# Kernel tuning notes

Hardware: AMD Instinct MI355X
Metric: run time of the kernel (lower is better)

The kernel has to match this reference:

```python
import jax, jax.numpy as jnp
import numpy as np
from jax import lax


def _batch_conv(x, w, b):
    # x: [B, Cin, H, W], w: [B, Cout, Cin, kh, kw], b: [B, Cout]
    # Per-sample conv (the torch code's groups=B grouped-conv trick),
    # expressed as vmap over the batch of an ordinary conv.
    def one(xi, wi):
        return lax.conv_general_dilated(
            xi[None], wi, window_strides=(1, 1), padding='SAME',
            dimension_numbers=('NCHW', 'OIHW', 'NCHW'))[0]
    y = jax.vmap(one)(x, w)                       # [B, Cout, H, W]
    return y + b[:, :, None, None]


def setup_inputs() -> dict:
    key = jax.random.key(0)
    ks = jax.random.split(key, 9)
    B, Cin, H, W = 32, 3, 64, 64
    NC = 10
    s = 0.05
    return {
        'x': jax.random.normal(ks[0], (B, Cin, H, W), jnp.float32),
        'conv1_weight': jax.random.normal(ks[1], (B, 64, Cin, 3, 3), jnp.float32) * s,
        'conv2_weight': jax.random.normal(ks[2], (B, 128, 64, 3, 3), jnp.float32) * s,
        'conv3_weight': jax.random.normal(ks[3], (B, 256, 128, 3, 3), jnp.float32) * s,
        'fc_weight': jax.random.normal(ks[4], (B, 1, NC), jnp.float32) * s,
        'bias1': jax.random.normal(ks[5], (B, 64), jnp.float32) * s,
        'bias2': jax.random.normal(ks[6], (B, 128), jnp.float32) * s,
        'bias3': jax.random.normal(ks[7], (B, 256), jnp.float32) * s,
        'bias4': jax.random.normal(ks[8], (B, NC), jnp.float32) * s,
    }


def reference(x, conv1_weight, conv2_weight, conv3_weight, fc_weight,
              bias1, bias2, bias3, bias4):
    h = jax.nn.relu(_batch_conv(x, conv1_weight, bias1))   # [B, 64, H, W]
    h = jax.nn.relu(_batch_conv(h, conv2_weight, bias2))   # [B, 128, H, W]
    h = jax.nn.relu(_batch_conv(h, conv3_weight, bias3))   # [B, 256, H, W]
    h = jnp.mean(h, axis=(2, 3))                           # AdaptiveAvgPool2d(1) -> [B, 256]
    h = h[:, :, None]                                      # view(B, N, -1) -> [B, 256, 1]
    # BatchLinearLayer: bmm(x, weight) + bias
    out = jnp.einsum('bnd,bdo->bno', h, fc_weight) + bias4[:, None, :]  # [B, 256, 10]
    return out
```

## Files before the change

### kernel.cpp

```cpp
#include <hip/hip_runtime.h>
#include <stdint.h>

typedef __attribute__((ext_vector_type(8))) short short8;
typedef __attribute__((ext_vector_type(16))) float f32x16;

#define NB 32

__device__ __forceinline__ float bf2f(uint16_t v) {
    return __uint_as_float(((uint32_t)v) << 16);
}
__device__ __forceinline__ uint16_t f2bf(float f) {
    uint32_t u = __float_as_uint(f);
    u += 0x7fffu + ((u >> 16) & 1u);
    return (uint16_t)(u >> 16);
}

__device__ __forceinline__ void gload16(const void* g, void* l) {
    __builtin_amdgcn_global_load_lds(
        (const __attribute__((address_space(1))) uint32_t*)g,
        (__attribute__((address_space(3))) uint32_t*)l, 16, 0, 0);
}

template<int COUT, int CIN>
__device__ __forceinline__ void prep_w_item(int idx, const float* __restrict__ w,
                                            uint16_t* __restrict__ wp)
{
    const int ci = idx % CIN;
    const int t  = idx / CIN;
    const int oc = t % COUT;
    const int b  = t / COUT;
    const float* s = w + (size_t)idx * 9;
    #pragma unroll
    for (int k = 0; k < 9; k++)
        wp[((size_t)(b * 9 + k) * COUT + oc) * CIN + ci] = f2bf(s[k]);
}

__global__ __launch_bounds__(256) void prep_w3_k(
    const float* __restrict__ w, uint16_t* __restrict__ wp)
{
    const int idx = blockIdx.x * 256 + threadIdx.x;
    if (idx < NB * 256 * 128) prep_w_item<256, 128>(idx, w, wp);
}

template<bool DO_W3>
__global__ __launch_bounds__(256) void prep_all(
    const float* __restrict__ x,  const float* __restrict__ w1,
    const float* __restrict__ w2, const float* __restrict__ w3,
    uint16_t* __restrict__ xp,  uint16_t* __restrict__ wp1,
    uint16_t* __restrict__ wp2, uint16_t* __restrict__ wp3,
    float* __restrict__ zp)
{
    int idx = blockIdx.x * 256 + threadIdx.x;
    if (idx < 4096) {
        ((float4*)zp)[idx] = make_float4(0.f, 0.f, 0.f, 0.f);
        return;
    }
    idx -= 4096;
    if (idx < 131072) {
        const int xc = idx & 63, y = (idx >> 6) & 63, b = idx >> 12;
        const float* s = x + (size_t)b * 3 * 4096 + y * 64 + xc;
        const uint16_t v0 = f2bf(s[0]), v1 = f2bf(s[4096]), v2 = f2bf(s[8192]);
        short8 lo = {(short)v0, (short)v1, (short)v2, 0, 0, 0, 0, 0};
        short8 hi = {0, 0, 0, 0, 0, 0, 0, 0};
        uint16_t* d = xp + (size_t)idx * 16;
        *(short8*)d = lo;
        *(short8*)(d + 8) = hi;
        return;
    }
    idx -= 131072;
    if (idx < 18432) {
        const int oc = idx & 63, k = (idx >> 6) % 9, b = idx / 576;
        const uint16_t v0 = f2bf(w1[((size_t)(b * 64 + oc) * 3 + 0) * 9 + k]);
        const uint16_t v1 = f2bf(w1[((size_t)(b * 64 + oc) * 3 + 1) * 9 + k]);
        const uint16_t v2 = f2bf(w1[((size_t)(b * 64 + oc) * 3 + 2) * 9 + k]);
        short8 lo = {(short)v0, (short)v1, (short)v2, 0, 0, 0, 0, 0};
        short8 hi = {0, 0, 0, 0, 0, 0, 0, 0};
        uint16_t* d = wp1 + ((size_t)(b * 9 + k) * 64 + oc) * 16;
        *(short8*)d = lo;
        *(short8*)(d + 8) = hi;
        return;
    }
    idx -= 18432;
    if (idx < 262144) {
        prep_w_item<128, 64>(idx, w2, wp2);
        return;
    }
    if (!DO_W3) return;
    idx -= 262144;
    if (idx < 1048576) prep_w_item<256, 128>(idx, w3, wp3);
}

template<int CIN, int COUT, int OCBLKS, bool POOL>
__global__ __launch_bounds__(512, 4) void conv_mfma(
    const uint16_t* __restrict__ in, const uint16_t* __restrict__ wp,
    const float* __restrict__ bias, uint16_t* __restrict__ out,
    float* __restrict__ partial, const float* __restrict__ zp)
{
    constexpr int IN_CH = 21;
    constexpr int W_CH  = 18;
    constexpr int IN_B  = IN_CH * 1024;
    constexpr int BUF_B = IN_B + W_CH * 1024;
    constexpr int P     = OCBLKS * 8;
    extern __shared__ __align__(16) char sm[];

    const int L   = blockIdx.x;
    const int xcd = L & 7;
    const int jj  = L >> 3;
    const int b   = (jj / P) * 8 + xcd;
    const int inner = jj % P;
    const int ocbase = (inner >> 3) * 64;
    const int stripe = inner & 7;
    const int y0 = stripe * 8;

    const int tid = threadIdx.x;
    const int w  = tid >> 6;
    const int wv = w >> 1, h = w & 1;
    const int l  = tid & 63, q = l >> 5, ln = l & 31;
    const int NK = CIN / 16;

    const uint16_t* srcp[5];
    int ldsoff[5];
    #pragma unroll
    for (int j = 0; j < 5; j++) {
        const int chunk = w * 5 + j;
        if (chunk >= IN_CH + W_CH) {
            srcp[j] = (const uint16_t*)zp;
            ldsoff[j] = -1;
        } else if (chunk < IN_CH) {
            const int gp = chunk * 64 + l;
            const int rq = gp / 66, px = gp - rq * 66;
            const int row = rq >> 1, qq = rq & 1;
            const int gy = y0 - 1 + row, gx = px - 1;
            const bool valid = (rq < 20) && ((unsigned)gy < 64u) && ((unsigned)gx < 64u);
            srcp[j] = valid ? in + ((size_t)((b * 64 + gy) * 64 + gx) * CIN + qq * 8)
                            : (const uint16_t*)zp;
            ldsoff[j] = chunk * 1024;
        } else {
            const int c2 = chunk - IN_CH;
            const int kk = c2 >> 1, qq = c2 & 1, oc = l;
            srcp[j] = wp + ((size_t)(b * 9 + kk) * COUT + ocbase + oc) * CIN + qq * 8;
            ldsoff[j] = IN_B + c2 * 1024;
        }
    }

    int aoffA[4];
    #pragma unroll
    for (int t = 0; t < 4; t++)
        aoffA[t] = ((((wv * 2 + t) * 2 + q) * 66) + h * 32 + ln) * 16;
    const int boffB = q * 1024 + ln * 16;

    f32x16 aA0, aA1, aC0, aC1;
    {
        const float bv0 = bias[b * COUT + ocbase + ln];
        const float bv1 = bias[b * COUT + ocbase + 32 + ln];
        #pragma unroll
        for (int r = 0; r < 16; r++) {
            aA0[r] = bv0; aC0[r] = bv0;
            aA1[r] = bv1; aC1[r] = bv1;
        }
    }

    auto stage = [&](int bufsel, int k) {
        const int koff = k * 16;
        char* base = sm + bufsel * BUF_B;
        #pragma unroll
        for (int j = 0; j < 5; j++) {
            char* dst = (ldsoff[j] < 0) ? (sm + 2 * BUF_B)
                                        : (base + ldsoff[j]);
            gload16(srcp[j] + koff, dst);
        }
    };

    stage(0, 0);
    if (NK > 1) stage(1, 1);

    for (int k = 0; k < NK; k++) {
        const char* cb = sm + (k & 1) * BUF_B;
        if (k + 1 < NK) asm volatile("s_waitcnt vmcnt(5)" ::: "memory");
        else            asm volatile("s_waitcnt vmcnt(0)" ::: "memory");
        __builtin_amdgcn_s_barrier();
        __builtin_amdgcn_sched_barrier(0);
        __builtin_amdgcn_s_setprio(1);
        #pragma unroll
        for (int kx = 0; kx < 3; kx++) {
            short8 fA[4];
            #pragma unroll
            for (int t = 0; t < 4; t++)
                fA[t] = *(const short8*)(cb + aoffA[t] + kx * 16);
            #pragma unroll
            for (int ky = 0; ky < 3; ky++) {
                const int kk = ky * 3 + kx;
                const char* bw = cb + IN_B + kk * 2048 + boffB;
                short8 b0 = *(const short8*)(bw);
                short8 b1 = *(const short8*)(bw + 512);
                aA0 = __builtin_amdgcn_mfma_f32_32x32x16_bf16(fA[ky], b0, aA0, 0, 0, 0);
                aA1 = __builtin_amdgcn_mfma_f32_32x32x16_bf16(fA[ky], b1, aA1, 0, 0, 0);
                aC0 = __builtin_amdgcn_mfma_f32_32x32x16_bf16(fA[ky + 1], b0, aC0, 0, 0, 0);
                aC1 = __builtin_amdgcn_mfma_f32_32x32x16_bf16(fA[ky + 1], b1, aC1, 0, 0, 0);
            }
        }
        __builtin_amdgcn_s_setprio(0);
        __builtin_amdgcn_s_barrier();
        if (k + 2 < NK) stage(k & 1, k + 2);
    }

    if (!POOL) {
        #pragma unroll
        for (int r = 0; r < 16; r++) {
            const int pxr = h * 32 + (r & 3) + 8 * (r >> 2) + 4 * q;
            const int y0w = y0 + wv * 2;
            uint16_t* dA = out + (size_t)((b * 64 + y0w) * 64 + pxr) * COUT + ocbase;
            uint16_t* dC = out + (size_t)((b * 64 + y0w + 1) * 64 + pxr) * COUT + ocbase;
            dA[ln]      = f2bf(fmaxf(aA0[r], 0.f));
            dA[32 + ln] = f2bf(fmaxf(aA1[r], 0.f));
            dC[ln]      = f2bf(fmaxf(aC0[r], 0.f));
            dC[32 + ln] = f2bf(fmaxf(aC1[r], 0.f));
        }
    } else {
        float* red = (float*)(sm + 2 * BUF_B);
        float s0 = 0.f, s1 = 0.f;
        #pragma unroll
        for (int r = 0; r < 16; r++) {
            s0 += fmaxf(aA0[r], 0.f) + fmaxf(aC0[r], 0.f);
            s1 += fmaxf(aA1[r], 0.f) + fmaxf(aC1[r], 0.f);
        }
        s0 += __shfl_xor(s0, 32);
        s1 += __shfl_xor(s1, 32);
        __syncthreads();
        if (q == 0) {
            red[w * 64 + ln] = s0;
            red[w * 64 + 32 + ln] = s1;
        }
        __syncthreads();
        if (tid < 64) {
            float t = 0.f;
            #pragma unroll
            for (int i = 0; i < 8; i++) t += red[i * 64 + tid];
            partial[(size_t)(b * 256 + ocbase + tid) * 8 + stripe] = t;
        }
    }
}

__global__ void fc_k(const float* __restrict__ partial,
                     const float* __restrict__ fcw,
                     const float* __restrict__ b4, float* __restrict__ out)
{
    const int b = blockIdx.x, c = threadIdx.x;
    const float* p = partial + (size_t)(b * 256 + c) * 8;
    float s = 0.f;
    #pragma unroll
    for (int i = 0; i < 8; i++) s += p[i];
    const float pooled = s * (1.f / 4096.f);
    #pragma unroll
    for (int o = 0; o < 10; o++)
        out[(b * 256 + c) * 10 + o] = fmaf(pooled, fcw[b * 10 + o], b4[b * 10 + o]);
}

extern "C" void kernel_launch(void* const* d_in, const int* in_sizes, int n_in,
                              void* d_out, int out_size, void* d_ws, size_t ws_size,
                              hipStream_t stream)
{
    const float* x   = (const float*)d_in[0];
    const float* w1  = (const float*)d_in[1];
    const float* w2  = (const float*)d_in[2];
    const float* w3  = (const float*)d_in[3];
    const float* fcw = (const float*)d_in[4];
    const float* b1  = (const float*)d_in[5];
    const float* b2  = (const float*)d_in[6];
    const float* b3  = (const float*)d_in[7];
    const float* b4  = (const float*)d_in[8];
    char* ws = (char*)d_ws;
    uint16_t* xp  = (uint16_t*)(ws);
    uint16_t* wp1 = (uint16_t*)(ws + 4194304);
    uint16_t* h2  = (uint16_t*)(ws);
    uint16_t* h1  = (uint16_t*)(ws + 33554432);
    uint16_t* wp2 = (uint16_t*)(ws + 50331648);
    const bool big_ws = ws_size >= 74186752u;
    uint16_t* wp3     = (uint16_t*)(ws + (big_ws ? 55050240u : 33554432u));
    float*    partial = (float*)   (ws + (big_ws ? 73924608u : 52428800u));
    float*    zp      = (float*)d_out;

    constexpr int DYN_LDS = 2 * 39936 + 2048;
    static bool attr_done = false;
    if (!attr_done) {
        hipFuncSetAttribute((const void*)&conv_mfma<16, 64, 1, false>,
                            hipFuncAttributeMaxDynamicSharedMemorySize, DYN_LDS);
        hipFuncSetAttribute((const void*)&conv_mfma<64, 128, 2, false>,
                            hipFuncAttributeMaxDynamicSharedMemorySize, DYN_LDS);
        hipFuncSetAttribute((const void*)&conv_mfma<128, 256, 4, true>,
                            hipFuncAttributeMaxDynamicSharedMemorySize, DYN_LDS);
        attr_done = true;
    }

    if (big_ws) {
        prep_all<true><<<5720, 256, 0, stream>>>(x, w1, w2, w3, xp, wp1, wp2, wp3, zp);
    } else {
        prep_all<false><<<1624, 256, 0, stream>>>(x, w1, w2, w3, xp, wp1, wp2, wp3, zp);
    }
    conv_mfma<16, 64, 1, false><<<NB * 8, 512, DYN_LDS, stream>>>(xp, wp1, b1, h1, nullptr, zp);
    conv_mfma<64, 128, 2, false><<<NB * 16, 512, DYN_LDS, stream>>>(h1, wp2, b2, h2, nullptr, zp);
    if (!big_ws)
        prep_w3_k<<<4096, 256, 0, stream>>>(w3, wp3);
    conv_mfma<128, 256, 4, true><<<NB * 32, 512, DYN_LDS, stream>>>(h2, wp3, b3, nullptr, partial, zp);
    fc_k<<<NB, 256, 0, stream>>>(partial, fcw, b4, (float*)d_out);
}
```

Before: 133.8 us.

## Retile conv kernels so each block covers all output channels of a 4-row stripe

The conv kernel is restructured so each 256-thread block computes every output channel for a 4-row stripe, instead of a 64-channel slice of an 8-row stripe. Each wave now holds a 4xNF grid of MFMA accumulators, which gives more reuse of each A and B fragment per LDS read. The K loop now walks (ky, channel-chunk) phases with smaller double-buffered LDS tiles, and the next kx fragments are prefetched into registers. This aims to cut redundant input loads across channel blocks and raise MFMA density. The cost is fewer blocks and waves per CU (launch_bounds 256,1), much higher register pressure for NF=4, and a per-phase full vmcnt(0) wait with a barrier.

```diff
diff --git a/kernel.cpp b/kernel.cpp
--- a/kernel.cpp
+++ b/kernel.cpp
@@ -6,9 +6,6 @@
 
 #define NB 32
 
-__device__ __forceinline__ float bf2f(uint16_t v) {
-    return __uint_as_float(((uint32_t)v) << 16);
-}
 __device__ __forceinline__ uint16_t f2bf(float f) {
     uint32_t u = __float_as_uint(f);
     u += 0x7fffu + ((u >> 16) & 1u);
@@ -90,153 +87,186 @@
     if (idx < 1048576) prep_w_item<256, 128>(idx, w3, wp3);
 }
 
-template<int CIN, int COUT, int OCBLKS, bool POOL>
-__global__ __launch_bounds__(512, 4) void conv_mfma(
+template<int CIN, int COUT, int NF, bool POOL>
+__global__ __launch_bounds__(256, 1) void conv_mfma(
     const uint16_t* __restrict__ in, const uint16_t* __restrict__ wp,
     const float* __restrict__ bias, uint16_t* __restrict__ out,
     float* __restrict__ partial, const float* __restrict__ zp)
 {
-    constexpr int IN_CH = 21;
-    constexpr int W_CH  = 18;
-    constexpr int IN_B  = IN_CH * 1024;
-    constexpr int BUF_B = IN_B + W_CH * 1024;
-    constexpr int P     = OCBLKS * 8;
+    constexpr int IN_B  = 9216;
+    constexpr int W_B   = NF * 6144;
+    constexpr int BUF_B = IN_B + W_B;
+    constexpr int TOT   = 9 + NF * 6;
+    constexpr int CPW   = (TOT + 3) / 4;
+    constexpr int NP    = 3 * (CIN / 16);
+    constexpr int NW64  = NF * 64;
     extern __shared__ __align__(16) char sm[];
 
     const int L   = blockIdx.x;
     const int xcd = L & 7;
     const int jj  = L >> 3;
-    const int b   = (jj / P) * 8 + xcd;
-    const int inner = jj % P;
-    const int ocbase = (inner >> 3) * 64;
-    const int stripe = inner & 7;
-    const int y0 = stripe * 8;
+    const int b   = (jj >> 4) * 8 + xcd;
+    const int stripe = jj & 15;
+    const int y0 = stripe * 4;
 
     const int tid = threadIdx.x;
-    const int w  = tid >> 6;
-    const int wv = w >> 1, h = w & 1;
-    const int l  = tid & 63, q = l >> 5, ln = l & 31;
-    const int NK = CIN / 16;
-
-    const uint16_t* srcp[5];
-    int ldsoff[5];
-    #pragma unroll
-    for (int j = 0; j < 5; j++) {
-        const int chunk = w * 5 + j;
-        if (chunk >= IN_CH + W_CH) {
-            srcp[j] = (const uint16_t*)zp;
+    const int w = tid >> 6, l = tid & 63, q = l >> 5, ln = l & 31;
+    const int wvM = w >> 1, wvN = w & 1;
+
+    const uint16_t* cptr[CPW];
+    int ldsoff[CPW];
+    int gy0a[CPW];
+    bool isin[CPW], vpx[CPW];
+    #pragma unroll
+    for (int j = 0; j < CPW; j++) {
+        const int chunk = w * CPW + j;
+        isin[j] = false; vpx[j] = false; gy0a[j] = 0;
+        if (chunk >= TOT) {
+            cptr[j] = (const uint16_t*)zp;
             ldsoff[j] = -1;
-        } else if (chunk < IN_CH) {
-            const int gp = chunk * 64 + l;
-            const int rq = gp / 66, px = gp - rq * 66;
-            const int row = rq >> 1, qq = rq & 1;
-            const int gy = y0 - 1 + row, gx = px - 1;
-            const bool valid = (rq < 20) && ((unsigned)gy < 64u) && ((unsigned)gx < 64u);
-            srcp[j] = valid ? in + ((size_t)((b * 64 + gy) * 64 + gx) * CIN + qq * 8)
-                            : (const uint16_t*)zp;
+        } else if (chunk < 9) {
+            const int gi = chunk * 64 + l;
+            const int rq = gi / 66, px = gi - rq * 66;
+            const int t = rq >> 1, qq = rq & 1;
+            const int gx = px - 1;
+            isin[j] = true;
+            vpx[j] = (gi < 528) && ((unsigned)gx < 64u);
+            gy0a[j] = y0 - 1 + t;
+            cptr[j] = in + ((size_t)(b * 64) * 64 + gx) * CIN + qq * 8;
             ldsoff[j] = chunk * 1024;
         } else {
-            const int c2 = chunk - IN_CH;
-            const int kk = c2 >> 1, qq = c2 & 1, oc = l;
-            srcp[j] = wp + ((size_t)(b * 9 + kk) * COUT + ocbase + oc) * CIN + qq * 8;
-            ldsoff[j] = IN_B + c2 * 1024;
+            const int wgi = (chunk - 9) * 64 + l;
+            const int kx = wgi / (NF * 128);
+            const int qq = (wgi / NW64) & 1;
+            const int oc = wgi % NW64;
+            cptr[j] = wp + ((size_t)(b * 9 + kx) * COUT + oc) * CIN + qq * 8;
+            ldsoff[j] = IN_B + (chunk - 9) * 1024;
         }
     }
 
     int aoffA[4];
     #pragma unroll
-    for (int t = 0; t < 4; t++)
-        aoffA[t] = ((((wv * 2 + t) * 2 + q) * 66) + h * 32 + ln) * 16;
-    const int boffB = q * 1024 + ln * 16;
-
-    f32x16 aA0, aA1, aC0, aC1;
+    for (int dh = 0; dh < 4; dh++) {
+        const int dr = dh >> 1, h = dh & 1;
+        const int t = wvM * 2 + dr;
+        aoffA[dh] = ((t * 2 + q) * 66 + h * 32 + ln) * 16;
+    }
+    int bbase[NF];
+    #pragma unroll
+    for (int n = 0; n < NF; n++)
+        bbase[n] = IN_B + (q * NW64 + wvN * (NF * 32) + n * 32 + ln) * 16;
+
+    f32x16 acc[4][NF];
     {
-        const float bv0 = bias[b * COUT + ocbase + ln];
-        const float bv1 = bias[b * COUT + ocbase + 32 + ln];
-        #pragma unroll
-        for (int r = 0; r < 16; r++) {
-            aA0[r] = bv0; aC0[r] = bv0;
-            aA1[r] = bv1; aC1[r] = bv1;
-        }
-    }
-
-    auto stage = [&](int bufsel, int k) {
-        const int koff = k * 16;
+        #pragma unroll
+        for (int n = 0; n < NF; n++) {
+            const float bv = bias[b * COUT + wvN * (NF * 32) + n * 32 + ln];
+            #pragma unroll
+            for (int dh = 0; dh < 4; dh++)
+                #pragma unroll
+                for (int r = 0; r < 16; r++) acc[dh][n][r] = bv;
+        }
+    }
+
+    auto stage = [&](int bufsel, int p) {
+        const int ky = p % 3, c = p / 3;
+        const size_t woff = (size_t)(3 * ky) * COUT * CIN + c * 16;
         char* base = sm + bufsel * BUF_B;
         #pragma unroll
-        for (int j = 0; j < 5; j++) {
-            char* dst = (ldsoff[j] < 0) ? (sm + 2 * BUF_B)
-                                        : (base + ldsoff[j]);
-            gload16(srcp[j] + koff, dst);
+        for (int j = 0; j < CPW; j++) {
+            const uint16_t* src;
+            char* dst;
+            if (ldsoff[j] < 0) {
+                src = (const uint16_t*)zp; dst = sm + 2 * BUF_B;
+            } else if (isin[j]) {
+                const int gy = gy0a[j] + ky;
+                const bool v = vpx[j] && ((unsigned)gy < 64u);
+                src = v ? cptr[j] + (size_t)gy * (64 * CIN) + c * 16
+                        : (const uint16_t*)zp;
+                dst = base + ldsoff[j];
+            } else {
+                src = cptr[j] + woff; dst = base + ldsoff[j];
+            }
+            gload16(src, dst);
         }
     };
 
     stage(0, 0);
-    if (NK > 1) stage(1, 1);
-
-    for (int k = 0; k < NK; k++) {
-        const char* cb = sm + (k & 1) * BUF_B;
-        if (k + 1 < NK) asm volatile("s_waitcnt vmcnt(5)" ::: "memory");
-        else            asm volatile("s_waitcnt vmcnt(0)" ::: "memory");
-        __builtin_amdgcn_s_barrier();
-        __builtin_amdgcn_sched_barrier(0);
+    asm volatile("s_waitcnt vmcnt(0)" ::: "memory");
+    __syncthreads();
+
+    for (int p = 0; p < NP; p++) {
+        const char* cb = sm + (p & 1) * BUF_B;
+        if (p + 1 < NP) stage((p + 1) & 1, p + 1);
+
+        short8 cA[4], cB[NF], nA[4], nB[NF];
+        #pragma unroll
+        for (int dh = 0; dh < 4; dh++)
+            cA[dh] = *(const short8*)(cb + aoffA[dh]);
+        #pragma unroll
+        for (int n = 0; n < NF; n++)
+            cB[n] = *(const short8*)(cb + bbase[n]);
         __builtin_amdgcn_s_setprio(1);
         #pragma unroll
         for (int kx = 0; kx < 3; kx++) {
-            short8 fA[4];
+            if (kx < 2) {
+                #pragma unroll
+                for (int dh = 0; dh < 4; dh++)
+                    nA[dh] = *(const short8*)(cb + aoffA[dh] + (kx + 1) * 16);
+                #pragma unroll
+                for (int n = 0; n < NF; n++)
+                    nB[n] = *(const short8*)(cb + bbase[n] + (kx + 1) * (NF * 2048));
+            }
+            __builtin_amdgcn_sched_barrier(0);
             #pragma unroll
-            for (int t = 0; t < 4; t++)
-                fA[t] = *(const short8*)(cb + aoffA[t] + kx * 16);
+            for (int dh = 0; dh < 4; dh++)
+                #pragma unroll
+                for (int n = 0; n < NF; n++)
+                    acc[dh][n] = __builtin_amdgcn_mfma_f32_32x32x16_bf16(
+                        cA[dh], cB[n], acc[dh][n], 0, 0, 0);
+            if (kx < 2) {
+                #pragma unroll
+                for (int dh = 0; dh < 4; dh++) cA[dh] = nA[dh];
+                #pragma unroll
+                for (int n = 0; n < NF; n++) cB[n] = nB[n];
+            }
+        }
+        __builtin_amdgcn_s_setprio(0);
+        asm volatile("s_waitcnt vmcnt(0)" ::: "memory");
+        __syncthreads();
+    }
+
+    if (!POOL) {
+        #pragma unroll
+        for (int dh = 0; dh < 4; dh++) {
+            const int dr = dh >> 1, h = dh & 1;
+            const int row = y0 + wvM * 2 + dr;
             #pragma unroll
-            for (int ky = 0; ky < 3; ky++) {
-                const int kk = ky * 3 + kx;
-                const char* bw = cb + IN_B + kk * 2048 + boffB;
-                short8 b0 = *(const short8*)(bw);
-                short8 b1 = *(const short8*)(bw + 512);
-                aA0 = __builtin_amdgcn_mfma_f32_32x32x16_bf16(fA[ky], b0, aA0, 0, 0, 0);
-                aA1 = __builtin_amdgcn_mfma_f32_32x32x16_bf16(fA[ky], b1, aA1, 0, 0, 0);
-                aC0 = __builtin_amdgcn_mfma_f32_32x32x16_bf16(fA[ky + 1], b0, aC0, 0, 0, 0);
-                aC1 = __builtin_amdgcn_mfma_f32_32x32x16_bf16(fA[ky + 1], b1, aC1, 0, 0, 0);
+            for (int r = 0; r < 16; r++) {
+                const int px = h * 32 + (r & 3) + 8 * (r >> 2) + 4 * q;
+                uint16_t* d = out + (size_t)((b * 64 + row) * 64 + px) * COUT
+                              + wvN * (NF * 32);
+                #pragma unroll
+                for (int n = 0; n < NF; n++)
+                    d[n * 32 + ln] = f2bf(fmaxf(acc[dh][n][r], 0.f));
             }
-        }
-        __builtin_amdgcn_s_setprio(0);
-        __builtin_amdgcn_s_barrier();
-        if (k + 2 < NK) stage(k & 1, k + 2);
-    }
-
-    if (!POOL) {
-        #pragma unroll
-        for (int r = 0; r < 16; r++) {
-            const int pxr = h * 32 + (r & 3) + 8 * (r >> 2) + 4 * q;
-            const int y0w = y0 + wv * 2;
-            uint16_t* dA = out + (size_t)((b * 64 + y0w) * 64 + pxr) * COUT + ocbase;
-            uint16_t* dC = out + (size_t)((b * 64 + y0w + 1) * 64 + pxr) * COUT + ocbase;
-            dA[ln]      = f2bf(fmaxf(aA0[r], 0.f));
-            dA[32 + ln] = f2bf(fmaxf(aA1[r], 0.f));
-            dC[ln]      = f2bf(fmaxf(aC0[r], 0.f));
-            dC[32 + ln] = f2bf(fmaxf(aC1[r], 0.f));
         }
     } else {
         float* red = (float*)(sm + 2 * BUF_B);
-        float s0 = 0.f, s1 = 0.f;
-        #pragma unroll
-        for (int r = 0; r < 16; r++) {
-            s0 += fmaxf(aA0[r], 0.f) + fmaxf(aC0[r], 0.f);
-            s1 += fmaxf(aA1[r], 0.f) + fmaxf(aC1[r], 0.f);
-        }
-        s0 += __shfl_xor(s0, 32);
-        s1 += __shfl_xor(s1, 32);
+        #pragma unroll
+        for (int n = 0; n < NF; n++) {
+            float s = 0.f;
+            #pragma unroll
+            for (int dh = 0; dh < 4; dh++)
+                #pragma unroll
+                for (int r = 0; r < 16; r++) s += fmaxf(acc[dh][n][r], 0.f);
+            s += __shfl_xor(s, 32);
+            if (q == 0) red[wvM * NW64 + wvN * (NF * 32) + n * 32 + ln] = s;
+        }
         __syncthreads();
-        if (q == 0) {
-            red[w * 64 + ln] = s0;
-            red[w * 64 + 32 + ln] = s1;
-        }
-        __syncthreads();
-        if (tid < 64) {
-            float t = 0.f;
-            #pragma unroll
-            for (int i = 0; i < 8; i++) t += red[i * 64 + tid];
-            partial[(size_t)(b * 256 + ocbase + tid) * 8 + stripe] = t;
+        if (tid < NW64) {
+            float t = red[tid] + red[NW64 + tid];
+            partial[(size_t)(b * COUT + tid) * 16 + stripe] = t;
         }
     }
 }
@@ -246,10 +276,10 @@
                      const float* __restrict__ b4, float* __restrict__ out)
 {
     const int b = blockIdx.x, c = threadIdx.x;
-    const float* p = partial + (size_t)(b * 256 + c) * 8;
+    const float* p = partial + (size_t)(b * 256 + c) * 16;
     float s = 0.f;
     #pragma unroll
-    for (int i = 0; i < 8; i++) s += p[i];
+    for (int i = 0; i < 16; i++) s += p[i];
     const float pooled = s * (1.f / 4096.f);
     #pragma unroll
     for (int o = 0; o < 10; o++)
@@ -275,20 +305,22 @@
     uint16_t* h2  = (uint16_t*)(ws);
     uint16_t* h1  = (uint16_t*)(ws + 33554432);
     uint16_t* wp2 = (uint16_t*)(ws + 50331648);
-    const bool big_ws = ws_size >= 74186752u;
+    const bool big_ws = ws_size >= 74448896u;
     uint16_t* wp3     = (uint16_t*)(ws + (big_ws ? 55050240u : 33554432u));
     float*    partial = (float*)   (ws + (big_ws ? 73924608u : 52428800u));
     float*    zp      = (float*)d_out;
 
-    constexpr int DYN_LDS = 2 * 39936 + 2048;
+    constexpr int DYN1 = 2 * (9216 + 1 * 6144) + 2048;
+    constexpr int DYN2 = 2 * (9216 + 2 * 6144) + 2048;
+    constexpr int DYN4 = 2 * (9216 + 4 * 6144) + 2048;
     static bool attr_done = false;
     if (!attr_done) {
         hipFuncSetAttribute((const void*)&conv_mfma<16, 64, 1, false>,
-                            hipFuncAttributeMaxDynamicSharedMemorySize, DYN_LDS);
+                            hipFuncAttributeMaxDynamicSharedMemorySize, DYN1);
         hipFuncSetAttribute((const void*)&conv_mfma<64, 128, 2, false>,
-                            hipFuncAttributeMaxDynamicSharedMemorySize, DYN_LDS);
+                            hipFuncAttributeMaxDynamicSharedMemorySize, DYN2);
         hipFuncSetAttribute((const void*)&conv_mfma<128, 256, 4, true>,
-                            hipFuncAttributeMaxDynamicSharedMemorySize, DYN_LDS);
+                            hipFuncAttributeMaxDynamicSharedMemorySize, DYN4);
         attr_done = true;
     }
 
@@ -297,10 +329,10 @@
     } else {
         prep_all<false><<<1624, 256, 0, stream>>>(x, w1, w2, w3, xp, wp1, wp2, wp3, zp);
     }
-    conv_mfma<16, 64, 1, false><<<NB * 8, 512, DYN_LDS, stream>>>(xp, wp1, b1, h1, nullptr, zp);
-    conv_mfma<64, 128, 2, false><<<NB * 16, 512, DYN_LDS, stream>>>(h1, wp2, b2, h2, nullptr, zp);
+    conv_mfma<16, 64, 1, false><<<NB * 16, 256, DYN1, stream>>>(xp, wp1, b1, h1, nullptr, zp);
+    conv_mfma<64, 128, 2, false><<<NB * 16, 256, DYN2, stream>>>(h1, wp2, b2, h2, nullptr, zp);
     if (!big_ws)
         prep_w3_k<<<4096, 256, 0, stream>>>(w3, wp3);
-    conv_mfma<128, 256, 4, true><<<NB * 32, 512, DYN_LDS, stream>>>(h2, wp3, b3, nullptr, partial, zp);
+    conv_mfma<128, 256, 4, true><<<NB * 16, 256, DYN4, stream>>>(h2, wp3, b3, nullptr, partial, zp);
     fc_k<<<NB, 256, 0, stream>>>(partial, fcw, b4, (float*)d_out);
 }
```

After: 175.6 us. 1.31x slower.
